# Kernel tuning notes

Hardware: AMD Instinct MI355X
Metric: run time of the kernel (lower is better)

Reference implementation:

```python
import jax, jax.numpy as jnp
import numpy as np

EMBED = 1024
HEADS = 16
HEAD_DIM = EMBED // HEADS


def setup_inputs() -> dict:
    key = jax.random.key(0)
    ks = jax.random.split(key, 9)
    B, S = 2, 2048
    values = jax.random.normal(ks[0], (B, S, EMBED), dtype=jnp.float32)
    keys_in = jax.random.normal(ks[1], (B, S, EMBED), dtype=jnp.float32)
    query = jax.random.normal(ks[2], (B, S, EMBED), dtype=jnp.float32)
    mask = jax.random.randint(ks[3], (B, 1, 1, S), 0, 2, dtype=jnp.int32)
    # torch Linear weights: [out_features, in_features], y = x @ W.T
    sc = 1.0 / np.sqrt(HEAD_DIM)
    Wv = jax.random.uniform(ks[4], (HEAD_DIM, HEAD_DIM), jnp.float32, -sc, sc)
    Wk = jax.random.uniform(ks[5], (HEAD_DIM, HEAD_DIM), jnp.float32, -sc, sc)
    Wq = jax.random.uniform(ks[6], (HEAD_DIM, HEAD_DIM), jnp.float32, -sc, sc)
    so = 1.0 / np.sqrt(EMBED)
    Wo = jax.random.uniform(ks[7], (EMBED, EMBED), jnp.float32, -so, so)
    bo = jax.random.uniform(ks[8], (EMBED,), jnp.float32, -so, so)
    return {"values": values, "keys": keys_in, "query": query, "mask": mask,
            "Wv": Wv, "Wk": Wk, "Wq": Wq, "Wo": Wo, "bo": bo}


def reference(values, keys, query, mask, Wv, Wk, Wq, Wo, bo):
    B = query.shape[0]
    # split heads: [B, S, H, D]
    v = values.reshape(B, -1, HEADS, HEAD_DIM)
    k = keys.reshape(B, -1, HEADS, HEAD_DIM)
    q = query.reshape(B, -1, HEADS, HEAD_DIM)
    # per-head shared linear projections (nn.Linear on last dim, no bias)
    v = jnp.einsum('bshd,ed->bshe', v, Wv)
    k = jnp.einsum('bshd,ed->bshe', k, Wk)
    q = jnp.einsum('bshd,ed->bshe', q, Wq)
    # energy: [B, H, Q, K]
    energy = jnp.einsum('bqhd,bkhd->bhqk', q, k)
    energy = jnp.where(mask == 0, jnp.float32(-1e20), energy)
    attn = jax.nn.softmax(energy / jnp.sqrt(jnp.float32(EMBED)), axis=3)
    out = jnp.einsum('bhqk,bkhd->bqhd', attn, v).reshape(B, -1, EMBED)
    return out @ Wo.T + bo
```

## Files before the change

### kernel.cpp

```cpp
#include <hip/hip_runtime.h>
#include <hip/hip_bf16.h>


typedef __attribute__((ext_vector_type(8))) short bf16x8;
typedef __attribute__((ext_vector_type(4))) float f32x4;
typedef __attribute__((ext_vector_type(16))) float f32x16;
typedef __attribute__((ext_vector_type(2))) int i32x2;

__device__ int g_srcidx[2 * 2048];
__device__ int g_NK[2];

__device__ __forceinline__ short f2bf(float x) {
  union { float f; unsigned u; } v; v.f = x;
  unsigned r = v.u + 0x7FFFu + ((v.u >> 16) & 1u);
  return (short)(r >> 16);
}

__device__ __forceinline__ int pack2(float lo, float hi) {
  __hip_bfloat162 h = __float22bfloat162_rn(make_float2(lo, hi));
  int r; __builtin_memcpy(&r, &h, 4); return r;
}

__device__ __forceinline__ bf16x8 cvt8(float4 a, float4 b) {
  union { int i[4]; bf16x8 h; } u;
  u.i[0] = pack2(a.x, a.y);
  u.i[1] = pack2(a.z, a.w);
  u.i[2] = pack2(b.x, b.y);
  u.i[3] = pack2(b.z, b.w);
  return u.h;
}

__device__ __forceinline__ void plsw(int& a, int& b) {
  i32x2 r = __builtin_amdgcn_permlane32_swap(a, b, false, false);
  a = r[0]; b = r[1];
}
__device__ __forceinline__ float pl_comb_add(float v) {
  int a = __float_as_int(v), b = a;
  i32x2 r = __builtin_amdgcn_permlane32_swap(a, b, false, false);
  return __int_as_float(r[0]) + __int_as_float(r[1]);
}

__device__ __forceinline__ void gll16(const short* g, short* l) {
  __builtin_amdgcn_global_load_lds(
      (const __attribute__((address_space(1))) void*)g,
      (__attribute__((address_space(3))) void*)l, 16, 0, 0);
}

__global__ __launch_bounds__(256) void prep_kernel(const int* __restrict__ mask) {
  __shared__ int cnt[256];
  const int t = threadIdx.x;
  const int b = blockIdx.x;
  const int* m = mask + b * 2048;
  int* sidx = g_srcidx + b * 2048;
  const int base = t * 8;
  int vals[8], lc = 0;
#pragma unroll
  for (int i = 0; i < 8; i++) { vals[i] = (m[base + i] != 0); lc += vals[i]; }
  cnt[t] = lc;
  __syncthreads();
  for (int off = 1; off < 256; off <<= 1) {
    int v = (t >= off) ? cnt[t - off] : 0;
    __syncthreads();
    cnt[t] += v;
    __syncthreads();
  }
  int pos = cnt[t] - lc;
  const int total = cnt[255];
#pragma unroll
  for (int i = 0; i < 8; i++)
    if (vals[i]) sidx[pos++] = base + i;
  for (int j = total + t; j < 2048; j += 256) sidx[j] = 0;
  if (t == 0) g_NK[b] = total;
}

__global__ __launch_bounds__(256) void proj_kernel(
    const float* __restrict__ keys, const float* __restrict__ query,
    const float* __restrict__ values,
    const float* __restrict__ Wk, const float* __restrict__ Wq,
    const float* __restrict__ Wv, const float* __restrict__ Wo,
    short* __restrict__ Kp, short* __restrict__ Qp, short* __restrict__ Vt,
    short* __restrict__ WoB) {
  const int bid0 = blockIdx.x;
  const int t = threadIdx.x;
  if (bid0 >= 3072) {
    int i = ((bid0 - 3072) * 256 + t) * 8;
    float4 a = *(const float4*)(Wo + i), b2 = *(const float4*)(Wo + i + 4);
    *(bf16x8*)(WoB + i) = cvt8(a, b2);
    return;
  }
  const int w = t >> 6, l = t & 63, l15 = l & 15, l4 = l >> 4;
  __shared__ short Al[64 * 64];
  __shared__ short Bl[64 * 64];
  __shared__ short Tl[64 * 66];

  if (bid0 < 2048) {
    int bid = bid0;
    const float* X = keys; const float* W = Wk; short* O = Kp;
    bool isq = false;
    if (bid >= 1024) { X = query; W = Wq; O = Qp; bid -= 1024; isq = true; }
    const int r0 = bid << 6;
    const int bb = r0 >> 15;
    if (!isq) {
      const int j0 = (r0 >> 4) & 2047;
      const int jlim = (g_NK[bb] + 63) & ~63;
      if (j0 >= jlim) return;
    }
#pragma unroll
    for (int i = 0; i < 2; i++) {
      int c = t + (i << 8);
      int row = c >> 3, col8 = c & 7;
      int pc = col8 ^ (row & 7);
      int ri = r0 + row;
      int j = (ri >> 4) & 2047, hh = ri & 15;
      int s = isq ? j : g_srcidx[(bb << 11) + j];
      const float* xs = X + ((size_t)((bb * 2048 + s) * 16 + hh)) * 64 + col8 * 8;
      float4 a0 = *(const float4*)xs, a1 = *(const float4*)(xs + 4);
      *(bf16x8*)&Al[row * 64 + pc * 8] = cvt8(a0, a1);
      const float* wsrc = W + row * 64 + col8 * 8;
      float4 b0 = *(const float4*)wsrc, b1 = *(const float4*)(wsrc + 4);
      *(bf16x8*)&Bl[row * 64 + pc * 8] = cvt8(b0, b1);
    }
    __syncthreads();
    f32x4 acc[4];
#pragma unroll
    for (int i = 0; i < 4; i++) acc[i] = (f32x4){0.f, 0.f, 0.f, 0.f};
#pragma unroll
    for (int kc = 0; kc < 2; kc++) {
      int ar = w * 16 + l15;
      bf16x8 af = *(const bf16x8*)((const char*)Al +
          ((ar * 128 + kc * 64 + l4 * 16) ^ ((ar & 7) << 4)));
#pragma unroll
      for (int ng = 0; ng < 4; ng++) {
        int br = ng * 16 + l15;
        bf16x8 bfr = *(const bf16x8*)((const char*)Bl +
            ((br * 128 + kc * 64 + l4 * 16) ^ ((br & 7) << 4)));
        acc[ng] = __builtin_amdgcn_mfma_f32_16x16x32_bf16(af, bfr, acc[ng], 0, 0, 0);
      }
    }
    const float osc = isq ? (1.4426950408889634f / 32.0f) : 1.0f;
#pragma unroll
    for (int ng = 0; ng < 4; ng++) {
#pragma unroll
      for (int j = 0; j < 4; j++) {
        int ri = r0 + w * 16 + l4 * 4 + j;
        int e = ng * 16 + l15;
        int b2 = ri >> 15, jj = (ri >> 4) & 2047, hh = ri & 15;
        O[(((size_t)(b2 * 16 + hh)) * 2048 + jj) * 64 + e] = f2bf(acc[ng][j] * osc);
      }
    }
  } else {
    const int bid = bid0 - 2048;
    const int st = bid & 31, bh = bid >> 5;
    const int b = bh >> 4, h = bh & 15;
    const int s0 = st << 6;
    const int jlim = (g_NK[b] + 63) & ~63;
    if (s0 >= jlim) return;
#pragma unroll
    for (int i = 0; i < 2; i++) {
      int c = t + (i << 8);
      int row = c >> 3, col8 = c & 7;
      int pc = col8 ^ (row & 7);
      int s = g_srcidx[(b << 11) + s0 + row];
      const float* xs = values + ((size_t)(b * 2048 + s)) * 1024 + h * 64 + col8 * 8;
      float4 a0 = *(const float4*)xs, a1 = *(const float4*)(xs + 4);
      *(bf16x8*)&Al[row * 64 + pc * 8] = cvt8(a0, a1);
      const float* wsrc = Wv + row * 64 + col8 * 8;
      float4 b0 = *(const float4*)wsrc, b1 = *(const float4*)(wsrc + 4);
      *(bf16x8*)&Bl[row * 64 + pc * 8] = cvt8(b0, b1);
    }
    __syncthreads();
    f32x4 acc[4];
#pragma unroll
    for (int i = 0; i < 4; i++) acc[i] = (f32x4){0.f, 0.f, 0.f, 0.f};
#pragma unroll
    for (int kc = 0; kc < 2; kc++) {
      int ar = w * 16 + l15;
      bf16x8 af = *(const bf16x8*)((const char*)Al +
          ((ar * 128 + kc * 64 + l4 * 16) ^ ((ar & 7) << 4)));
#pragma unroll
      for (int ng = 0; ng < 4; ng++) {
        int br = ng * 16 + l15;
        bf16x8 bfr = *(const bf16x8*)((const char*)Bl +
            ((br * 128 + kc * 64 + l4 * 16) ^ ((br & 7) << 4)));
        acc[ng] = __builtin_amdgcn_mfma_f32_16x16x32_bf16(af, bfr, acc[ng], 0, 0, 0);
      }
    }
#pragma unroll
    for (int ng = 0; ng < 4; ng++) {
#pragma unroll
      for (int j = 0; j < 4; j++) {
        Tl[(w * 16 + l4 * 4 + j) * 66 + ng * 16 + l15] = f2bf(acc[ng][j]);
      }
    }
    __syncthreads();
    int e = t >> 2, sc = (t & 3) << 4;
    bf16x8 o0, o1;
#pragma unroll
    for (int i = 0; i < 8; i++) {
      o0[i] = Tl[(sc + i) * 66 + e];
      o1[i] = Tl[(sc + 8 + i) * 66 + e];
    }
    short* dst = Vt + ((size_t)bh * 64 + e) * 2048 + s0 + sc;
    *(bf16x8*)dst = o0;
    *(bf16x8*)(dst + 8) = o1;
  }
}

__global__ __launch_bounds__(256, 2) void attn_kernel(
    const short* __restrict__ Qp, const short* __restrict__ Kp,
    const short* __restrict__ Vt, short* __restrict__ AO) {
  const int bid = (int)(blockIdx.x % 8) * 64 + (int)(blockIdx.x / 8);
  const int qb = bid & 15, bh = bid >> 4;
  const int b = bh >> 4, h = bh & 15;
  const int t = threadIdx.x;
  const int w = t >> 6, l = t & 63, l31 = l & 31, hi = l >> 5;
  const int q0w = qb * 128 + w * 32;

  __shared__ short Kl[2][64 * 64];
  __shared__ short Vl[2][64 * 64];
  __shared__ float Cl[4 * 32];

  const short* Kbase = Kp + (size_t)bh * 2048 * 64;
  const short* Vbase = Vt + (size_t)bh * 64 * 2048;

  const int nk = g_NK[b];
  const int ntiles = (nk + 63) >> 6;

  const short* qptr = Qp + ((size_t)bh * 2048 + q0w + l31) * 64 + hi * 8;
  bf16x8 qf[4];
#pragma unroll
  for (int dc = 0; dc < 4; dc++) qf[dc] = *(const bf16x8*)(qptr + dc * 16);

  int laddr[2][4];
#pragma unroll
  for (int x = 0; x < 2; x++) {
    int rr = x * 32 + l31;
#pragma unroll
    for (int c2 = 0; c2 < 4; c2++)
      laddr[x][c2] = rr * 128 + (((c2 * 32) + hi * 16) ^ ((rr & 7) << 4));
  }

  const int srow = t >> 3, scol = t & 7;
  const int sc0 = (scol ^ (srow & 7)) * 8;
  const short* ksrc0 = Kbase + srow * 64 + sc0;
  const short* ksrc1 = Kbase + (srow + 32) * 64 + sc0;
  const short* vsrc0 = Vbase + (size_t)srow * 2048 + sc0;
  const short* vsrc1 = Vbase + (size_t)(srow + 32) * 2048 + sc0;
  short* klds = &Kl[0][0];
  short* vlds = &Vl[0][0];
  const int d0 = t * 8, d1 = t * 8 + 2048;

  gll16(ksrc0, klds + d0);
  gll16(ksrc1, klds + d1);
  gll16(vsrc0, vlds + d0);
  gll16(vsrc1, vlds + d1);
  __syncthreads();

  float sxa[8];
#pragma unroll
  for (int i = 0; i < 8; i++) sxa[i] = 0.f;
  f32x16 o0, o1;
#pragma unroll
  for (int r = 0; r < 16; r++) { o0[r] = 0.f; o1[r] = 0.f; }

  for (int kt = 0; kt < ntiles; kt++) {
    const int bs = kt & 1;
    const int bsb = bs << 13;
    if (kt + 1 < ntiles) {
      const int nb = (bs ^ 1) << 12;
      gll16(ksrc0 + (kt + 1) * 4096, klds + nb + d0);
      gll16(ksrc1 + (kt + 1) * 4096, klds + nb + d1);
      gll16(vsrc0 + (kt + 1) * 64, vlds + nb + d0);
      gll16(vsrc1 + (kt + 1) * 64, vlds + nb + d1);
    }

    f32x16 st0, st1;
#pragma unroll
    for (int r = 0; r < 16; r++) { st0[r] = 0.f; st1[r] = 0.f; }
    __builtin_amdgcn_s_setprio(1);
#pragma unroll
    for (int dc = 0; dc < 4; dc++) {
      bf16x8 ka = *(const bf16x8*)((const char*)Kl + bsb + laddr[0][dc]);
      st0 = __builtin_amdgcn_mfma_f32_32x32x16_bf16(ka, qf[dc], st0, 0, 0, 0);
    }
#pragma unroll
    for (int dc = 0; dc < 4; dc++) {
      bf16x8 kb = *(const bf16x8*)((const char*)Kl + bsb + laddr[1][dc]);
      st1 = __builtin_amdgcn_mfma_f32_32x32x16_bf16(kb, qf[dc], st1, 0, 0, 0);
    }
    __builtin_amdgcn_s_setprio(0);

    if (((kt << 6) + 64) <= nk) {
#pragma unroll
      for (int r = 0; r < 16; r++) {
        st0[r] = __builtin_amdgcn_exp2f(st0[r]);
        st1[r] = __builtin_amdgcn_exp2f(st1[r]);
      }
    } else {
      const int kb2 = kt << 6;
#pragma unroll
      for (int r = 0; r < 16; r++) {
        int cr = (r & 3) + 8 * (r >> 2) + 4 * hi;
        float e0 = __builtin_amdgcn_exp2f(st0[r]);
        float e1 = __builtin_amdgcn_exp2f(st1[r]);
        st0[r] = (kb2 + cr < nk) ? e0 : 0.f;
        st1[r] = (kb2 + 32 + cr < nk) ? e1 : 0.f;
      }
    }

#pragma unroll
    for (int i = 0; i < 8; i++)
      sxa[i] += (st0[2 * i] + st0[2 * i + 1]) + (st1[2 * i] + st1[2 * i + 1]);

    bf16x8 pa[4];
#pragma unroll
    for (int kc = 0; kc < 4; kc++) {
      int bse = (kc & 1) * 8;
      float p0, p1, p2, p3, p4, p5, p6, p7;
      if (kc < 2) {
        p0 = st0[bse + 0]; p1 = st0[bse + 1]; p2 = st0[bse + 2]; p3 = st0[bse + 3];
        p4 = st0[bse + 4]; p5 = st0[bse + 5]; p6 = st0[bse + 6]; p7 = st0[bse + 7];
      } else {
        p0 = st1[bse + 0]; p1 = st1[bse + 1]; p2 = st1[bse + 2]; p3 = st1[bse + 3];
        p4 = st1[bse + 4]; p5 = st1[bse + 5]; p6 = st1[bse + 6]; p7 = st1[bse + 7];
      }
      int A0 = pack2(p0, p1), A1 = pack2(p2, p3);
      int B0 = pack2(p4, p5), B1 = pack2(p6, p7);
      plsw(A0, B0);
      plsw(A1, B1);
      union { int4 i; bf16x8 h; } u;
      u.i = make_int4(A0, A1, B0, B1);
      pa[kc] = u.h;
    }

    __builtin_amdgcn_s_setprio(1);
#pragma unroll
    for (int kc = 0; kc < 4; kc++) {
      bf16x8 vf = *(const bf16x8*)((const char*)Vl + bsb + laddr[0][kc]);
      o0 = __builtin_amdgcn_mfma_f32_32x32x16_bf16(pa[kc], vf, o0, 0, 0, 0);
    }
#pragma unroll
    for (int kc = 0; kc < 4; kc++) {
      bf16x8 vf = *(const bf16x8*)((const char*)Vl + bsb + laddr[1][kc]);
      o1 = __builtin_amdgcn_mfma_f32_32x32x16_bf16(pa[kc], vf, o1, 0, 0, 0);
    }
    __builtin_amdgcn_s_setprio(0);
    __syncthreads();
  }

#pragma unroll
  for (int s2 = 4; s2 > 0; s2 >>= 1)
#pragma unroll
    for (int i = 0; i < 4; i++)
      if (i < s2) sxa[i] += sxa[i + s2];
  float l_run = pl_comb_add(sxa[0]);

  float invr = 1.0f / l_run;
  Cl[w * 32 + l31] = invr;
  short* aob = AO + ((size_t)(b * 2048 + q0w)) * 1024 + h * 64 + l31;
#pragma unroll
  for (int r = 0; r < 16; r++) {
    int qr = (r & 3) + 8 * (r >> 2) + 4 * hi;
    float ic = Cl[w * 32 + qr];
    aob[(size_t)qr * 1024] = f2bf(o0[r] * ic);
    aob[(size_t)qr * 1024 + 32] = f2bf(o1[r] * ic);
  }
}

__global__ __launch_bounds__(512) void outproj_kernel(
    const short* __restrict__ AO, const short* __restrict__ WoB,
    const float* __restrict__ bo, float* __restrict__ Cout) {
  const int bid = (int)(blockIdx.x % 8) * 32 + (int)(blockIdx.x / 8);
  const int mt = bid >> 3, nt = bid & 7;
  const int m0 = mt << 7, n0 = nt << 7;
  const int t = threadIdx.x;
  const int w = t >> 6, wr = w >> 2, wc = w & 3;
  const int l = t & 63, l15 = l & 15, l4 = l >> 4;
  __shared__ short Al[2][128 * 64];
  __shared__ short Bl[2][128 * 64];

  const short* asrc[2];
  const short* bsrc[2];
  int ldst[2];
#pragma unroll
  for (int i = 0; i < 2; i++) {
    int c = t + (i << 9);
    int row = c >> 3, col8 = c & 7;
    int sc = (col8 ^ (row & 7)) * 8;
    asrc[i] = AO + (size_t)(m0 + row) * 1024 + sc;
    bsrc[i] = WoB + (size_t)(n0 + row) * 1024 + sc;
    ldst[i] = c * 8;
  }
  short* al = &Al[0][0];
  short* bl = &Bl[0][0];

  auto stage = [&](int ks, int bs) {
    const int nb = bs << 13;
    const int ko = ks * 64;
#pragma unroll
    for (int i = 0; i < 2; i++) {
      gll16(asrc[i] + ko, al + nb + ldst[i]);
      gll16(bsrc[i] + ko, bl + nb + ldst[i]);
    }
  };

  stage(0, 0);
  __syncthreads();

  f32x4 acc[4][2];
#pragma unroll
  for (int mi = 0; mi < 4; mi++)
#pragma unroll
    for (int ni = 0; ni < 2; ni++) acc[mi][ni] = (f32x4){0.f, 0.f, 0.f, 0.f};

  for (int ks = 0; ks < 16; ks++) {
    const int bs = ks & 1, bsb = bs << 14;
    if (ks < 15) stage(ks + 1, bs ^ 1);
#pragma unroll
    for (int kc = 0; kc < 2; kc++) {
      bf16x8 af[4];
#pragma unroll
      for (int mi = 0; mi < 4; mi++) {
        int ar = wr * 64 + mi * 16 + l15;
        af[mi] = *(const bf16x8*)((const char*)Al + bsb +
            ((ar * 128 + kc * 64 + l4 * 16) ^ ((ar & 7) << 4)));
      }
#pragma unroll
      for (int ni = 0; ni < 2; ni++) {
        int br = wc * 32 + ni * 16 + l15;
        bf16x8 bfr = *(const bf16x8*)((const char*)Bl + bsb +
            ((br * 128 + kc * 64 + l4 * 16) ^ ((br & 7) << 4)));
#pragma unroll
        for (int mi = 0; mi < 4; mi++)
          acc[mi][ni] = __builtin_amdgcn_mfma_f32_16x16x32_bf16(
              af[mi], bfr, acc[mi][ni], 0, 0, 0);
      }
    }
    __syncthreads();
  }

#pragma unroll
  for (int ni = 0; ni < 2; ni++) {
    int n = n0 + wc * 32 + ni * 16 + l15;
    float bias = bo[n];
#pragma unroll
    for (int mi = 0; mi < 4; mi++) {
#pragma unroll
      for (int j = 0; j < 4; j++) {
        int m = m0 + wr * 64 + mi * 16 + l4 * 4 + j;
        Cout[(size_t)m * 1024 + n] = acc[mi][ni][j] + bias;
      }
    }
  }
}

extern "C" void kernel_launch(void* const* d_in, const int* in_sizes, int n_in,
                              void* d_out, int out_size, void* d_ws, size_t ws_size,
                              hipStream_t stream) {
  const float* values = (const float*)d_in[0];
  const float* keys   = (const float*)d_in[1];
  const float* query  = (const float*)d_in[2];
  const int*   mask   = (const int*)d_in[3];
  const float* Wv = (const float*)d_in[4];
  const float* Wk = (const float*)d_in[5];
  const float* Wq = (const float*)d_in[6];
  const float* Wo = (const float*)d_in[7];
  const float* bo = (const float*)d_in[8];
  float* out = (float*)d_out;
  char* ws = (char*)d_ws;
  short* Qp  = (short*)(ws + (size_t)0);
  short* Kp  = (short*)(ws + ((size_t)8 << 20));
  short* Vtp = (short*)(ws + ((size_t)16 << 20));
  short* AO  = (short*)(ws + ((size_t)24 << 20));
  short* WoB = (short*)(ws + ((size_t)32 << 20));

  prep_kernel<<<2, 256, 0, stream>>>(mask);
  proj_kernel<<<3584, 256, 0, stream>>>(keys, query, values, Wk, Wq, Wv, Wo,
                                        Kp, Qp, Vtp, WoB);
  attn_kernel<<<512, 256, 0, stream>>>(Qp, Kp, Vtp, AO);
  outproj_kernel<<<256, 512, 0, stream>>>(AO, WoB, bo, out);
}
```

Baseline: 65.93 us.

## Software-pipeline attention loop: overlap QK of next tile with softmax-PV of previous

Switches the K/V shared-memory staging from double to triple buffering and restructures the key-tile loop as a two-stage software pipeline. The QK^T MFMAs for tile i are issued before the exp2, bf16 pack and PV MFMAs for tile i-1, using two alternating score register sets. The goal is to hide the latency of the exponential and conversion work behind matrix-core work. In exchange it uses 50% more LDS per block and extra VGPRs for the second score set, which could hurt occupancy under the 2-blocks-per-CU launch bound.

```diff
diff --git a/kernel.cpp b/kernel.cpp
--- a/kernel.cpp
+++ b/kernel.cpp
@@ -216,8 +216,8 @@
   const int w = t >> 6, l = t & 63, l31 = l & 31, hi = l >> 5;
   const int q0w = qb * 128 + w * 32;
 
-  __shared__ short Kl[2][64 * 64];
-  __shared__ short Vl[2][64 * 64];
+  __shared__ short Kl[3][64 * 64];
+  __shared__ short Vl[3][64 * 64];
   __shared__ float Cl[4 * 32];
 
   const short* Kbase = Kp + (size_t)bh * 2048 * 64;
@@ -250,11 +250,13 @@
   short* vlds = &Vl[0][0];
   const int d0 = t * 8, d1 = t * 8 + 2048;
 
-  gll16(ksrc0, klds + d0);
-  gll16(ksrc1, klds + d1);
-  gll16(vsrc0, vlds + d0);
-  gll16(vsrc1, vlds + d1);
-  __syncthreads();
+  auto stage = [&](int kt, int bufi) {
+    const int off = bufi << 12;
+    gll16(ksrc0 + kt * 4096, klds + off + d0);
+    gll16(ksrc1 + kt * 4096, klds + off + d1);
+    gll16(vsrc0 + kt * 64, vlds + off + d0);
+    gll16(vsrc1 + kt * 64, vlds + off + d1);
+  };
 
   float sxa[8];
 #pragma unroll
@@ -263,66 +265,55 @@
 #pragma unroll
   for (int r = 0; r < 16; r++) { o0[r] = 0.f; o1[r] = 0.f; }
 
-  for (int kt = 0; kt < ntiles; kt++) {
-    const int bs = kt & 1;
-    const int bsb = bs << 13;
-    if (kt + 1 < ntiles) {
-      const int nb = (bs ^ 1) << 12;
-      gll16(ksrc0 + (kt + 1) * 4096, klds + nb + d0);
-      gll16(ksrc1 + (kt + 1) * 4096, klds + nb + d1);
-      gll16(vsrc0 + (kt + 1) * 64, vlds + nb + d0);
-      gll16(vsrc1 + (kt + 1) * 64, vlds + nb + d1);
-    }
-
-    f32x16 st0, st1;
-#pragma unroll
-    for (int r = 0; r < 16; r++) { st0[r] = 0.f; st1[r] = 0.f; }
+  auto qk = [&](int bsb, f32x16& s0, f32x16& s1) {
+#pragma unroll
+    for (int r = 0; r < 16; r++) { s0[r] = 0.f; s1[r] = 0.f; }
     __builtin_amdgcn_s_setprio(1);
 #pragma unroll
     for (int dc = 0; dc < 4; dc++) {
       bf16x8 ka = *(const bf16x8*)((const char*)Kl + bsb + laddr[0][dc]);
-      st0 = __builtin_amdgcn_mfma_f32_32x32x16_bf16(ka, qf[dc], st0, 0, 0, 0);
+      s0 = __builtin_amdgcn_mfma_f32_32x32x16_bf16(ka, qf[dc], s0, 0, 0, 0);
     }
 #pragma unroll
     for (int dc = 0; dc < 4; dc++) {
       bf16x8 kb = *(const bf16x8*)((const char*)Kl + bsb + laddr[1][dc]);
-      st1 = __builtin_amdgcn_mfma_f32_32x32x16_bf16(kb, qf[dc], st1, 0, 0, 0);
+      s1 = __builtin_amdgcn_mfma_f32_32x32x16_bf16(kb, qf[dc], s1, 0, 0, 0);
     }
     __builtin_amdgcn_s_setprio(0);
-
+  };
+
+  auto finish = [&](int kt, int bsbv, f32x16& s0, f32x16& s1) {
     if (((kt << 6) + 64) <= nk) {
 #pragma unroll
       for (int r = 0; r < 16; r++) {
-        st0[r] = __builtin_amdgcn_exp2f(st0[r]);
-        st1[r] = __builtin_amdgcn_exp2f(st1[r]);
+        s0[r] = __builtin_amdgcn_exp2f(s0[r]);
+        s1[r] = __builtin_amdgcn_exp2f(s1[r]);
       }
     } else {
       const int kb2 = kt << 6;
 #pragma unroll
       for (int r = 0; r < 16; r++) {
         int cr = (r & 3) + 8 * (r >> 2) + 4 * hi;
-        float e0 = __builtin_amdgcn_exp2f(st0[r]);
-        float e1 = __builtin_amdgcn_exp2f(st1[r]);
-        st0[r] = (kb2 + cr < nk) ? e0 : 0.f;
-        st1[r] = (kb2 + 32 + cr < nk) ? e1 : 0.f;
-      }
-    }
-
+        float e0 = __builtin_amdgcn_exp2f(s0[r]);
+        float e1 = __builtin_amdgcn_exp2f(s1[r]);
+        s0[r] = (kb2 + cr < nk) ? e0 : 0.f;
+        s1[r] = (kb2 + 32 + cr < nk) ? e1 : 0.f;
+      }
+    }
 #pragma unroll
     for (int i = 0; i < 8; i++)
-      sxa[i] += (st0[2 * i] + st0[2 * i + 1]) + (st1[2 * i] + st1[2 * i + 1]);
-
+      sxa[i] += (s0[2 * i] + s0[2 * i + 1]) + (s1[2 * i] + s1[2 * i + 1]);
     bf16x8 pa[4];
 #pragma unroll
     for (int kc = 0; kc < 4; kc++) {
       int bse = (kc & 1) * 8;
       float p0, p1, p2, p3, p4, p5, p6, p7;
       if (kc < 2) {
-        p0 = st0[bse + 0]; p1 = st0[bse + 1]; p2 = st0[bse + 2]; p3 = st0[bse + 3];
-        p4 = st0[bse + 4]; p5 = st0[bse + 5]; p6 = st0[bse + 6]; p7 = st0[bse + 7];
+        p0 = s0[bse + 0]; p1 = s0[bse + 1]; p2 = s0[bse + 2]; p3 = s0[bse + 3];
+        p4 = s0[bse + 4]; p5 = s0[bse + 5]; p6 = s0[bse + 6]; p7 = s0[bse + 7];
       } else {
-        p0 = st1[bse + 0]; p1 = st1[bse + 1]; p2 = st1[bse + 2]; p3 = st1[bse + 3];
-        p4 = st1[bse + 4]; p5 = st1[bse + 5]; p6 = st1[bse + 6]; p7 = st1[bse + 7];
+        p0 = s1[bse + 0]; p1 = s1[bse + 1]; p2 = s1[bse + 2]; p3 = s1[bse + 3];
+        p4 = s1[bse + 4]; p5 = s1[bse + 5]; p6 = s1[bse + 6]; p7 = s1[bse + 7];
       }
       int A0 = pack2(p0, p1), A1 = pack2(p2, p3);
       int B0 = pack2(p4, p5), B1 = pack2(p6, p7);
@@ -332,27 +323,52 @@
       u.i = make_int4(A0, A1, B0, B1);
       pa[kc] = u.h;
     }
-
     __builtin_amdgcn_s_setprio(1);
 #pragma unroll
     for (int kc = 0; kc < 4; kc++) {
-      bf16x8 vf = *(const bf16x8*)((const char*)Vl + bsb + laddr[0][kc]);
+      bf16x8 vf = *(const bf16x8*)((const char*)Vl + bsbv + laddr[0][kc]);
       o0 = __builtin_amdgcn_mfma_f32_32x32x16_bf16(pa[kc], vf, o0, 0, 0, 0);
     }
 #pragma unroll
     for (int kc = 0; kc < 4; kc++) {
-      bf16x8 vf = *(const bf16x8*)((const char*)Vl + bsb + laddr[1][kc]);
+      bf16x8 vf = *(const bf16x8*)((const char*)Vl + bsbv + laddr[1][kc]);
       o1 = __builtin_amdgcn_mfma_f32_32x32x16_bf16(pa[kc], vf, o1, 0, 0, 0);
     }
     __builtin_amdgcn_s_setprio(0);
-    __syncthreads();
-  }
+  };
+
+  stage(0, 0);
+  if (ntiles > 1) stage(1, 1);
+  __syncthreads();
+  f32x16 sA0, sA1, sB0, sB1;
+  qk(0, sA0, sA1);
+
+  int prv = 0, cur = 1, nxt = 2;
+  int i = 1;
+  bool lastInA = true;
+  while (i < ntiles) {
+    if (i + 1 < ntiles) stage(i + 1, nxt);
+    qk(cur << 13, sB0, sB1);
+    finish(i - 1, prv << 13, sA0, sA1);
+    prv = cur; cur = nxt; nxt = (nxt == 2) ? 0 : nxt + 1;
+    __syncthreads();
+    i++;
+    if (i >= ntiles) { lastInA = false; break; }
+    if (i + 1 < ntiles) stage(i + 1, nxt);
+    qk(cur << 13, sA0, sA1);
+    finish(i - 1, prv << 13, sB0, sB1);
+    prv = cur; cur = nxt; nxt = (nxt == 2) ? 0 : nxt + 1;
+    __syncthreads();
+    i++;
+  }
+  if (lastInA) finish(ntiles - 1, prv << 13, sA0, sA1);
+  else         finish(ntiles - 1, prv << 13, sB0, sB1);
 
 #pragma unroll
   for (int s2 = 4; s2 > 0; s2 >>= 1)
 #pragma unroll
-    for (int i = 0; i < 4; i++)
-      if (i < s2) sxa[i] += sxa[i + s2];
+    for (int ii = 0; ii < 4; ii++)
+      if (ii < s2) sxa[ii] += sxa[ii + s2];
   float l_run = pl_comb_add(sxa[0]);
 
   float invr = 1.0f / l_run;
```

Result: slower. 70.31 us (+6.6%).

## Double attention block to 8 waves sharing K/V tiles across 256 queries

Applied to the files above, without the earlier changes.

Each attention block now processes 256 query rows with 8 waves instead of 128 rows with 4 waves. The grid halves to 256 blocks, and each K/V tile loaded into LDS is reused by twice as many waves. The load split changes so that half the threads fetch K and the other half fetch V. This cuts global and L2 traffic for K/V, but 256 blocks gives fewer blocks than before to fill the GPU's compute units, and the launch-bounds occupancy hint is dropped.

```diff
diff --git a/kernel.cpp b/kernel.cpp
--- a/kernel.cpp
+++ b/kernel.cpp
@@ -206,19 +206,19 @@
   }
 }
 
-__global__ __launch_bounds__(256, 2) void attn_kernel(
+__global__ __launch_bounds__(512) void attn_kernel(
     const short* __restrict__ Qp, const short* __restrict__ Kp,
     const short* __restrict__ Vt, short* __restrict__ AO) {
-  const int bid = (int)(blockIdx.x % 8) * 64 + (int)(blockIdx.x / 8);
-  const int qb = bid & 15, bh = bid >> 4;
+  const int bid = (int)(blockIdx.x % 8) * 32 + (int)(blockIdx.x / 8);
+  const int qb = bid & 7, bh = bid >> 3;
   const int b = bh >> 4, h = bh & 15;
   const int t = threadIdx.x;
   const int w = t >> 6, l = t & 63, l31 = l & 31, hi = l >> 5;
-  const int q0w = qb * 128 + w * 32;
+  const int q0w = qb * 256 + w * 32;
 
   __shared__ short Kl[2][64 * 64];
   __shared__ short Vl[2][64 * 64];
-  __shared__ float Cl[4 * 32];
+  __shared__ float Cl[8 * 32];
 
   const short* Kbase = Kp + (size_t)bh * 2048 * 64;
   const short* Vbase = Vt + (size_t)bh * 64 * 2048;
@@ -240,20 +240,26 @@
       laddr[x][c2] = rr * 128 + (((c2 * 32) + hi * 16) ^ ((rr & 7) << 4));
   }
 
-  const int srow = t >> 3, scol = t & 7;
+  const int sh = t >> 8, tt = t & 255;
+  const int srow = tt >> 3, scol = tt & 7;
   const int sc0 = (scol ^ (srow & 7)) * 8;
-  const short* ksrc0 = Kbase + srow * 64 + sc0;
-  const short* ksrc1 = Kbase + (srow + 32) * 64 + sc0;
-  const short* vsrc0 = Vbase + (size_t)srow * 2048 + sc0;
-  const short* vsrc1 = Vbase + (size_t)(srow + 32) * 2048 + sc0;
-  short* klds = &Kl[0][0];
-  short* vlds = &Vl[0][0];
-  const int d0 = t * 8, d1 = t * 8 + 2048;
-
-  gll16(ksrc0, klds + d0);
-  gll16(ksrc1, klds + d1);
-  gll16(vsrc0, vlds + d0);
-  gll16(vsrc1, vlds + d1);
+  const short* src0;
+  const short* src1;
+  short* dlds;
+  if (sh == 0) {
+    src0 = Kbase + srow * 64 + sc0;
+    src1 = Kbase + (srow + 32) * 64 + sc0;
+    dlds = &Kl[0][0];
+  } else {
+    src0 = Vbase + (size_t)srow * 2048 + sc0;
+    src1 = Vbase + (size_t)(srow + 32) * 2048 + sc0;
+    dlds = &Vl[0][0];
+  }
+  const int step0 = (sh == 0) ? 4096 : 64;
+  const int d0 = tt * 8, d1 = tt * 8 + 2048;
+
+  gll16(src0, dlds + d0);
+  gll16(src1, dlds + d1);
   __syncthreads();
 
   float sxa[8];
@@ -268,10 +274,8 @@
     const int bsb = bs << 13;
     if (kt + 1 < ntiles) {
       const int nb = (bs ^ 1) << 12;
-      gll16(ksrc0 + (kt + 1) * 4096, klds + nb + d0);
-      gll16(ksrc1 + (kt + 1) * 4096, klds + nb + d1);
-      gll16(vsrc0 + (kt + 1) * 64, vlds + nb + d0);
-      gll16(vsrc1 + (kt + 1) * 64, vlds + nb + d1);
+      gll16(src0 + (size_t)(kt + 1) * step0, dlds + nb + d0);
+      gll16(src1 + (size_t)(kt + 1) * step0, dlds + nb + d1);
     }
 
     f32x16 st0, st1;
@@ -477,6 +481,6 @@
   prep_kernel<<<2, 256, 0, stream>>>(mask);
   proj_kernel<<<3584, 256, 0, stream>>>(keys, query, values, Wk, Wq, Wv, Wo,
                                         Kp, Qp, Vtp, WoB);
-  attn_kernel<<<512, 256, 0, stream>>>(Qp, Kp, Vtp, AO);
+  attn_kernel<<<256, 512, 0, stream>>>(Qp, Kp, Vtp, AO);
   outproj_kernel<<<256, 512, 0, stream>>>(AO, WoB, bo, out);
 }
```

After: 64.90 us, median of 3. About the same (-1.6%).
